# Performance work log

Measured on AMD Instinct MI355X. Metric: run time of the kernel, lower is better.

## Reference

```python
import jax, jax.numpy as jnp
import numpy as np

N_NODES = 40000
N_EDGES = 640000
HIDDEN = 128


def setup_inputs() -> dict:
    key = jax.random.key(0)
    k1, k2, k3, k4 = jax.random.split(key, 4)
    x = jax.random.normal(k1, (N_NODES, HIDDEN), dtype=jnp.float32)
    edge_index = jax.random.randint(k2, (2, N_EDGES), 0, N_NODES, dtype=jnp.int64)
    # nn.Linear(2*hidden, 1): weight [1, 2*hidden], bias [1]
    bound = 1.0 / np.sqrt(2 * HIDDEN)
    att_w = jax.random.uniform(k3, (1, 2 * HIDDEN), minval=-bound, maxval=bound, dtype=jnp.float32)
    att_b = jax.random.uniform(k4, (1,), minval=-bound, maxval=bound, dtype=jnp.float32)
    eps = jnp.array([0.1], dtype=jnp.float32)
    return {"x": x, "edge_index": edge_index, "att_w": att_w, "att_b": att_b, "eps": eps}


def reference(x, edge_index, att_w, att_b, eps):
    d = x.shape[1]
    row, col = edge_index[0], edge_index[1]
    x_i = x[row]                               # [E, d]
    x_j = x[col]                               # [E, d]
    # att(cat([x_i, x_j])) == x_i @ w_i + x_j @ w_j + b  (avoids materializing concat)
    w = att_w[0]                               # [2d]
    logits = x_i @ w[:d] + x_j @ w[d:] + att_b[0]   # [E]
    alpha = jnp.tanh(logits)
    messages = alpha[:, None] * x_i            # [E, d]
    out = jax.ops.segment_sum(messages, col, num_segments=x.shape[0])  # scatter_add over col
    e = eps[0]
    return e * x + (1.0 - e) * out
```

## Files before the change

### kernel.cpp

```cpp
#include <hip/hip_runtime.h>
#include <hip/hip_fp16.h>
#include <math.h>


#define NHID 128
#define NNODES 40000
#define NEDGES 640000
#define CAP 64
#define CSTRIDE 16

__global__ __launch_bounds__(256) void node_pre_kernel(
    const float* __restrict__ x,
    const float* __restrict__ att_w,
    const float* __restrict__ att_b,
    float* __restrict__ s1,
    float* __restrict__ s2,
    __half* __restrict__ xh,
    int* __restrict__ cursor) {
    int gid = blockIdx.x * 256 + threadIdx.x;
    if (gid < NNODES * CSTRIDE / 16 * 16 && gid < 640000) cursor[gid] = 0;

    int lane = threadIdx.x & 63;
    int half = lane >> 5;
    int sub  = lane & 31;
    int node = blockIdx.x * 8 + (threadIdx.x >> 6) * 2 + half;
    if (node >= NNODES) return;

    float4 xv = ((const float4*)(x + (size_t)node * NHID))[sub];
    float4 w1 = ((const float4*)att_w)[sub];
    float4 w2 = ((const float4*)(att_w + NHID))[sub];

    __half2 h0; h0.x = __float2half_rn(xv.x); h0.y = __float2half_rn(xv.y);
    __half2 h1; h1.x = __float2half_rn(xv.z); h1.y = __float2half_rn(xv.w);
    uint2 hu;
    hu.x = *(unsigned*)&h0;
    hu.y = *(unsigned*)&h1;
    ((uint2*)(xh + (size_t)node * NHID))[sub] = hu;

    float p1 = xv.x * w1.x + xv.y * w1.y + xv.z * w1.z + xv.w * w1.w;
    float p2 = xv.x * w2.x + xv.y * w2.y + xv.z * w2.z + xv.w * w2.w;
#pragma unroll
    for (int off = 16; off > 0; off >>= 1) {
        p1 += __shfl_xor(p1, off, 64);
        p2 += __shfl_xor(p2, off, 64);
    }
    if (sub == 0) {
        s1[node] = p1;
        s2[node] = p2 + att_b[0];
    }
}

__global__ __launch_bounds__(256) void bucket_kernel(
    const int* __restrict__ ei,
    int* __restrict__ cursor,
    unsigned short* __restrict__ buck) {
    int e = blockIdx.x * 256 + threadIdx.x;
    if (e >= NEDGES) return;
    int r = ei[e];
    int c = ei[NEDGES + e];
    int pos = atomicAdd(&cursor[c * CSTRIDE], 1);
    if (pos < CAP) {
        buck[(size_t)c * CAP + pos] = (unsigned short)r;
    }
}

__device__ __forceinline__ void acc_edge(float4& acc, float a, uint2 u) {
    __half2 h0 = *(__half2*)&u.x;
    __half2 h1 = *(__half2*)&u.y;
    float2 f0 = __half22float2(h0);
    float2 f1 = __half22float2(h1);
    acc.x += a * f0.x; acc.y += a * f0.y;
    acc.z += a * f1.x; acc.w += a * f1.y;
}

__global__ __launch_bounds__(256) void gather_kernel(
    const float* __restrict__ x,
    const __half* __restrict__ xh,
    const float* __restrict__ s1,
    const float* __restrict__ s2,
    const float* __restrict__ eps,
    const int* __restrict__ cursor,
    const unsigned short* __restrict__ buck,
    float* __restrict__ out) {
    int lane = threadIdx.x & 63;
    int half = lane >> 5;
    int sub  = lane & 31;
    int hbase = lane & 32;
    int node = blockIdx.x * 8 + (threadIdx.x >> 6) * 2 + half;
    if (node >= NNODES) return;

    int cnt = cursor[node * CSTRIDE];
    cnt = (cnt < CAP) ? cnt : CAP;

    float e = eps[0];
    float coef = 1.0f - e;
    float s2n = s2[node];

    const unsigned short* bk = buck + (size_t)node * CAP;
    int   r0_l = (sub      < cnt) ? (int)bk[sub]      : 0;
    int   r1_l = (sub + 32 < cnt) ? (int)bk[sub + 32] : 0;
    float a0_l = (sub      < cnt) ? coef * tanhf(s1[r0_l] + s2n) : 0.0f;
    float a1_l = (sub + 32 < cnt) ? coef * tanhf(s1[r1_l] + s2n) : 0.0f;

    float4 xv = ((const float4*)(x + (size_t)node * NHID))[sub];
    float4 acc;
    acc.x = e * xv.x; acc.y = e * xv.y;
    acc.z = e * xv.z; acc.w = e * xv.w;

    int jmax = (cnt < 32) ? cnt : 32;
    int j = 0;
    for (; j + 4 <= jmax; j += 4) {
        int   q0 = __shfl(r0_l, hbase | (j + 0), 64);
        int   q1 = __shfl(r0_l, hbase | (j + 1), 64);
        int   q2 = __shfl(r0_l, hbase | (j + 2), 64);
        int   q3 = __shfl(r0_l, hbase | (j + 3), 64);
        uint2 u0 = ((const uint2*)(xh + (size_t)q0 * NHID))[sub];
        uint2 u1 = ((const uint2*)(xh + (size_t)q1 * NHID))[sub];
        uint2 u2 = ((const uint2*)(xh + (size_t)q2 * NHID))[sub];
        uint2 u3 = ((const uint2*)(xh + (size_t)q3 * NHID))[sub];
        float b0 = __shfl(a0_l, hbase | (j + 0), 64);
        float b1 = __shfl(a0_l, hbase | (j + 1), 64);
        float b2 = __shfl(a0_l, hbase | (j + 2), 64);
        float b3 = __shfl(a0_l, hbase | (j + 3), 64);
        acc_edge(acc, b0, u0);
        acc_edge(acc, b1, u1);
        acc_edge(acc, b2, u2);
        acc_edge(acc, b3, u3);
    }
    for (; j < jmax; j++) {
        int   q = __shfl(r0_l, hbase | j, 64);
        float b = __shfl(a0_l, hbase | j, 64);
        uint2 u = ((const uint2*)(xh + (size_t)q * NHID))[sub];
        acc_edge(acc, b, u);
    }
    for (int j2 = 32; j2 < cnt; j2++) {
        int   q = __shfl(r1_l, hbase | (j2 - 32), 64);
        float b = __shfl(a1_l, hbase | (j2 - 32), 64);
        uint2 u = ((const uint2*)(xh + (size_t)q * NHID))[sub];
        acc_edge(acc, b, u);
    }

    ((float4*)(out + (size_t)node * NHID))[sub] = acc;
}

extern "C" void kernel_launch(void* const* d_in, const int* in_sizes, int n_in,
                              void* d_out, int out_size, void* d_ws, size_t ws_size,
                              hipStream_t stream) {
    const float* x     = (const float*)d_in[0];
    const int*   ei    = (const int*)d_in[1];
    const float* att_w = (const float*)d_in[2];
    const float* att_b = (const float*)d_in[3];
    const float* eps   = (const float*)d_in[4];
    float* out = (float*)d_out;

    float*          s1     = (float*)d_ws;
    float*          s2     = s1 + NNODES;
    __half*         xh     = (__half*)(s2 + NNODES);
    int*            cursor = (int*)(xh + (size_t)NNODES * NHID);
    unsigned short* buck   = (unsigned short*)(cursor + NNODES * CSTRIDE);

    node_pre_kernel<<<NNODES / 8, 256, 0, stream>>>(
        x, att_w, att_b, s1, s2, xh, cursor);
    bucket_kernel<<<(NEDGES + 255) / 256, 256, 0, stream>>>(ei, cursor, buck);
    gather_kernel<<<NNODES / 8, 256, 0, stream>>>(
        x, xh, s1, s2, eps, cursor, buck, out);
}
```

Baseline: 136.5 us.

## Merge node preprocessing and edge bucketing into one interleaved kernel

```diff
diff --git a/kernel.cpp b/kernel.cpp
--- a/kernel.cpp
+++ b/kernel.cpp
@@ -9,64 +9,66 @@
 #define CAP 64
 #define CSTRIDE 16
 
-__global__ __launch_bounds__(256) void node_pre_kernel(
+__global__ __launch_bounds__(256) void zero_cursor_kernel(int* __restrict__ cursor) {
+    int gid = blockIdx.x * 256 + threadIdx.x;
+    if (gid < NNODES * CSTRIDE) cursor[gid] = 0;
+}
+
+__global__ __launch_bounds__(256) void pre_bucket_kernel(
     const float* __restrict__ x,
     const float* __restrict__ att_w,
     const float* __restrict__ att_b,
+    const int* __restrict__ ei,
     float* __restrict__ s1,
     float* __restrict__ s2,
     __half* __restrict__ xh,
-    int* __restrict__ cursor) {
-    int gid = blockIdx.x * 256 + threadIdx.x;
-    if (gid < NNODES * CSTRIDE / 16 * 16 && gid < 640000) cursor[gid] = 0;
-
-    int lane = threadIdx.x & 63;
-    int half = lane >> 5;
-    int sub  = lane & 31;
-    int node = blockIdx.x * 8 + (threadIdx.x >> 6) * 2 + half;
-    if (node >= NNODES) return;
-
-    float4 xv = ((const float4*)(x + (size_t)node * NHID))[sub];
-    float4 w1 = ((const float4*)att_w)[sub];
-    float4 w2 = ((const float4*)(att_w + NHID))[sub];
-
-    __half2 h0; h0.x = __float2half_rn(xv.x); h0.y = __float2half_rn(xv.y);
-    __half2 h1; h1.x = __float2half_rn(xv.z); h1.y = __float2half_rn(xv.w);
-    uint2 hu;
-    hu.x = *(unsigned*)&h0;
-    hu.y = *(unsigned*)&h1;
-    ((uint2*)(xh + (size_t)node * NHID))[sub] = hu;
-
-    float p1 = xv.x * w1.x + xv.y * w1.y + xv.z * w1.z + xv.w * w1.w;
-    float p2 = xv.x * w2.x + xv.y * w2.y + xv.z * w2.z + xv.w * w2.w;
-#pragma unroll
-    for (int off = 16; off > 0; off >>= 1) {
-        p1 += __shfl_xor(p1, off, 64);
-        p2 += __shfl_xor(p2, off, 64);
-    }
-    if (sub == 0) {
-        s1[node] = p1;
-        s2[node] = p2 + att_b[0];
-    }
-}
-
-__global__ __launch_bounds__(256) void bucket_kernel(
-    const int* __restrict__ ei,
     int* __restrict__ cursor,
     unsigned short* __restrict__ buck) {
-    int e = blockIdx.x * 256 + threadIdx.x;
-    if (e >= NEDGES) return;
-    int r = ei[e];
-    int c = ei[NEDGES + e];
-    int pos = atomicAdd(&cursor[c * CSTRIDE], 1);
-    if (pos < CAP) {
-        buck[(size_t)c * CAP + pos] = (unsigned short)r;
+    int g  = blockIdx.x / 3;
+    int r3 = blockIdx.x % 3;
+    if (r3 != 2) {
+        int nb   = g * 2 + r3;
+        int lane = threadIdx.x & 63;
+        int half = lane >> 5;
+        int sub  = lane & 31;
+        int node = nb * 8 + (threadIdx.x >> 6) * 2 + half;
+
+        float4 xv = ((const float4*)(x + (size_t)node * NHID))[sub];
+        float4 w1 = ((const float4*)att_w)[sub];
+        float4 w2 = ((const float4*)(att_w + NHID))[sub];
+
+        __half2 h0; h0.x = __float2half_rn(xv.x); h0.y = __float2half_rn(xv.y);
+        __half2 h1; h1.x = __float2half_rn(xv.z); h1.y = __float2half_rn(xv.w);
+        uint2 hu;
+        hu.x = __builtin_bit_cast(unsigned, h0);
+        hu.y = __builtin_bit_cast(unsigned, h1);
+        ((uint2*)(xh + (size_t)node * NHID))[sub] = hu;
+
+        float p1 = xv.x * w1.x + xv.y * w1.y + xv.z * w1.z + xv.w * w1.w;
+        float p2 = xv.x * w2.x + xv.y * w2.y + xv.z * w2.z + xv.w * w2.w;
+#pragma unroll
+        for (int off = 16; off > 0; off >>= 1) {
+            p1 += __shfl_xor(p1, off, 64);
+            p2 += __shfl_xor(p2, off, 64);
+        }
+        if (sub == 0) {
+            s1[node] = p1;
+            s2[node] = p2 + att_b[0];
+        }
+    } else {
+        int e = g * 256 + threadIdx.x;
+        int r = ei[e];
+        int c = ei[NEDGES + e];
+        int pos = atomicAdd(&cursor[c * CSTRIDE], 1);
+        if (pos < CAP) {
+            buck[(size_t)c * CAP + pos] = (unsigned short)r;
+        }
     }
 }
 
 __device__ __forceinline__ void acc_edge(float4& acc, float a, uint2 u) {
-    __half2 h0 = *(__half2*)&u.x;
-    __half2 h1 = *(__half2*)&u.y;
+    __half2 h0 = __builtin_bit_cast(__half2, u.x);
+    __half2 h1 = __builtin_bit_cast(__half2, u.y);
     float2 f0 = __half22float2(h0);
     float2 f1 = __half22float2(h1);
     acc.x += a * f0.x; acc.y += a * f0.y;
@@ -159,9 +161,9 @@
     int*            cursor = (int*)(xh + (size_t)NNODES * NHID);
     unsigned short* buck   = (unsigned short*)(cursor + NNODES * CSTRIDE);
 
-    node_pre_kernel<<<NNODES / 8, 256, 0, stream>>>(
-        x, att_w, att_b, s1, s2, xh, cursor);
-    bucket_kernel<<<(NEDGES + 255) / 256, 256, 0, stream>>>(ei, cursor, buck);
+    zero_cursor_kernel<<<(NNODES * CSTRIDE) / 256, 256, 0, stream>>>(cursor);
+    pre_bucket_kernel<<<7500, 256, 0, stream>>>(
+        x, att_w, att_b, ei, s1, s2, xh, cursor, buck);
     gather_kernel<<<NNODES / 8, 256, 0, stream>>>(
         x, xh, s1, s2, eps, cursor, buck, out);
 }
```

Result: no change. 138.7 us (+1.6%).
